# Performance work log

Measured on AMD Instinct MI355X. Metric: run time of the kernel, lower is better.

Reference implementation:

```python
import jax, jax.numpy as jnp
import numpy as np


def setup_inputs() -> dict:
    key = jax.random.key(0)
    kq, kk, kv = jax.random.split(key, 3)
    B, H, S, D = 2, 16, 2048, 64
    q = jax.random.normal(kq, (B, H, S, D), dtype=jnp.float32)
    k = jax.random.normal(kk, (B, H, S, D), dtype=jnp.float32)
    v = jax.random.normal(kv, (B, H, S, D), dtype=jnp.float32)
    return {"q": q, "k": k, "v": v}


def reference(q, k, v):
    # q,k,v: [B,H,S,D]; causal=True
    B, H, S, D = q.shape
    scale = D ** (-0.5)
    scores = jnp.einsum("bhsd,bhtd->bhst", q, k) * scale  # [B,H,S,S]
    causal_mask = jnp.triu(jnp.ones((S, S), dtype=bool), k=1)
    scores = jnp.where(causal_mask, -jnp.inf, scores)
    weights = jax.nn.softmax(scores, axis=-1)
    return jnp.einsum("bhst,bhtd->bhsd", weights, v)
```

## Files before the change

kernel.cpp:

```cpp
#include <hip/hip_runtime.h>
#include <hip/hip_bf16.h>


typedef unsigned int u32;
typedef unsigned short u16;
typedef unsigned long long u64;
typedef __attribute__((ext_vector_type(8))) short short8;
typedef __attribute__((ext_vector_type(4))) float f32x4;

#define DEV static __device__ __forceinline__

constexpr int S_ = 2048, D_ = 64;
constexpr int ELEMS = 2 * 16 * S_ * D_;
constexpr float SCL = 0.125f * 1.44269504089f;

DEV u16 f2bf(float f) {
  u32 u = __builtin_bit_cast(u32, f);
  u += 0x7fffu + ((u >> 16) & 1u);
  return (u16)(u >> 16);
}
DEV u32 pk2(float lo, float hi) { return (u32)f2bf(lo) | ((u32)f2bf(hi) << 16); }
DEV u64 pk4(float4 v) { return (u64)pk2(v.x, v.y) | ((u64)pk2(v.z, v.w) << 32); }

struct Q4 { u32 w[4]; };
struct P2 { u64 a, b; };

__global__ __launch_bounds__(256)
void convbf(const float* __restrict__ src, u16* __restrict__ dst, int n4) {
  int i = blockIdx.x * blockDim.x + threadIdx.x;
  const int stride = gridDim.x * blockDim.x;
  for (; i < n4; i += stride) {
    float4 v = ((const float4*)src)[i];
    ((u64*)dst)[i] = pk4(v);
  }
}

__global__ __launch_bounds__(256, 2)
void fattn(const float* __restrict__ Qg, const u16* __restrict__ Kbf,
           const u16* __restrict__ Vbf, float* __restrict__ Og)
{
  __shared__ __align__(16) u16 Kl[64 * 64];
  __shared__ __align__(16) u16 Vt[64 * 68];
  __shared__ __align__(16) u16 Pl[4][16 * 72];

  const int tid  = threadIdx.x;
  const int wid  = tid >> 6;
  const int lane = tid & 63;
  const int c    = lane & 15;
  const int g    = lane >> 4;

  const int n  = blockIdx.x;
  const int bh = n & 31;
  const int p  = n >> 5;
  const int qbs[2] = {31 - p, p};

  const float* Qb = Qg  + (size_t)bh * S_ * D_;
  const u16*   Kb = Kbf + (size_t)bh * S_ * D_;
  const u16*   Vb = Vbf + (size_t)bh * S_ * D_;
  float*       Ob = Og  + (size_t)bh * S_ * D_;

  char* Kbyte = (char*)Kl;
  char* Vbyte = (char*)Vt;
  char* Pbyte = (char*)(Pl[wid]);

  const int m16  = (tid & 7) * 16;
  const int rK0  = tid >> 3;
  const int rK1  = rK0 + 32;
  const int cf4  = tid & 15;
  const int d0   = cf4 * 4;
  const int kvl0 = 2 * (tid >> 4);
  const int kvl1 = kvl0 + 32;
  short8 pkA, pkB;
  u64 pva0, pvb0, pva1, pvb1;

#define ISSUE(T) do {                                                   \
    const u16* Kt_ = Kb + (size_t)(T) * 64 * D_;                        \
    const u16* Vg_ = Vb + (size_t)(T) * 64 * D_;                        \
    pkA  = *(const short8*)((const char*)Kt_ + rK0 * 128 + m16);        \
    pkB  = *(const short8*)((const char*)Kt_ + rK1 * 128 + m16);        \
    pva0 = *(const u64*)(Vg_ + (size_t)(kvl0    ) * D_ + d0);           \
    pvb0 = *(const u64*)(Vg_ + (size_t)(kvl0 + 1) * D_ + d0);           \
    pva1 = *(const u64*)(Vg_ + (size_t)(kvl1    ) * D_ + d0);           \
    pvb1 = *(const u64*)(Vg_ + (size_t)(kvl1 + 1) * D_ + d0);           \
  } while (0)

  ISSUE(0);

  for (int sp = 0; sp < 2; ++sp) {
    const int qb = qbs[sp];
    const int q0 = qb * 64;
    const int ntiles = qb + 1;

    const int qrow = q0 + wid * 16 + c;
    short8 qf[2];
    for (int kc = 0; kc < 2; ++kc) {
      const float* qp = Qb + (size_t)qrow * D_ + kc * 32 + 8 * g;
      float4 x = *(const float4*)qp;
      float4 y = *(const float4*)(qp + 4);
      Q4 q;
      q.w[0] = pk2(x.x * SCL, x.y * SCL);
      q.w[1] = pk2(x.z * SCL, x.w * SCL);
      q.w[2] = pk2(y.x * SCL, y.y * SCL);
      q.w[3] = pk2(y.z * SCL, y.w * SCL);
      qf[kc] = __builtin_bit_cast(short8, q);
    }

    f32x4 oa[4];
    for (int nd = 0; nd < 4; ++nd) oa[nd] = f32x4{0.f, 0.f, 0.f, 0.f};
    float mrow[4], lrow[4];
    for (int i = 0; i < 4; ++i) { mrow[i] = -__builtin_inff(); lrow[i] = 0.f; }

    for (int t = 0; t < ntiles; ++t) {
      const int kv0 = t * 64;
      __syncthreads();

      {
        *(short8*)(Kbyte + rK0 * 128 + (m16 ^ ((rK0 & 7) << 4))) = pkA;
        *(short8*)(Kbyte + rK1 * 128 + (m16 ^ ((rK1 & 7) << 4))) = pkB;
        u32 a0 = (u32)pva0, a1 = (u32)(pva0 >> 32);
        u32 b0 = (u32)pvb0, b1 = (u32)(pvb0 >> 32);
        *(u32*)(Vbyte + (d0 + 0) * 136 + kvl0 * 2) = (a0 & 0xffffu) | (b0 << 16);
        *(u32*)(Vbyte + (d0 + 1) * 136 + kvl0 * 2) = (a0 >> 16) | (b0 & 0xffff0000u);
        *(u32*)(Vbyte + (d0 + 2) * 136 + kvl0 * 2) = (a1 & 0xffffu) | (b1 << 16);
        *(u32*)(Vbyte + (d0 + 3) * 136 + kvl0 * 2) = (a1 >> 16) | (b1 & 0xffff0000u);
        a0 = (u32)pva1; a1 = (u32)(pva1 >> 32);
        b0 = (u32)pvb1; b1 = (u32)(pvb1 >> 32);
        *(u32*)(Vbyte + (d0 + 0) * 136 + kvl1 * 2) = (a0 & 0xffffu) | (b0 << 16);
        *(u32*)(Vbyte + (d0 + 1) * 136 + kvl1 * 2) = (a0 >> 16) | (b0 & 0xffff0000u);
        *(u32*)(Vbyte + (d0 + 2) * 136 + kvl1 * 2) = (a1 & 0xffffu) | (b1 << 16);
        *(u32*)(Vbyte + (d0 + 3) * 136 + kvl1 * 2) = (a1 >> 16) | (b1 & 0xffff0000u);
      }

      if (t + 1 < ntiles) ISSUE(t + 1);
      else if (sp == 0)   ISSUE(0);

      asm volatile("s_waitcnt lgkmcnt(0)" ::: "memory");
      __builtin_amdgcn_s_barrier();
      asm volatile("" ::: "memory");

      f32x4 sa[4];
      for (int nn = 0; nn < 4; ++nn) {
        sa[nn] = f32x4{0.f, 0.f, 0.f, 0.f};
        const int rowk = nn * 16 + c;
        const int base = rowk * 128;
        const int swz  = (rowk & 7) << 4;
        for (int kc = 0; kc < 2; ++kc) {
          short8 kf = *(const short8*)(Kbyte + base + ((kc * 64 + 16 * g) ^ swz));
          sa[nn] = __builtin_amdgcn_mfma_f32_16x16x32_bf16(qf[kc], kf, sa[nn], 0, 0, 0);
        }
      }

      const bool diag = (t == ntiles - 1);
      float pp[4][4];
      for (int i = 0; i < 4; ++i) {
        const int qg_ = q0 + wid * 16 + 4 * g + i;
        float s0v = sa[0][i], s1v = sa[1][i], s2v = sa[2][i], s3v = sa[3][i];
        if (diag) {
          if (kv0 +  0 + c > qg_) s0v = -__builtin_inff();
          if (kv0 + 16 + c > qg_) s1v = -__builtin_inff();
          if (kv0 + 32 + c > qg_) s2v = -__builtin_inff();
          if (kv0 + 48 + c > qg_) s3v = -__builtin_inff();
        }
        float mx = fmaxf(fmaxf(s0v, s1v), fmaxf(s2v, s3v));
        mx = fmaxf(mx, __shfl_xor(mx, 1));
        mx = fmaxf(mx, __shfl_xor(mx, 2));
        mx = fmaxf(mx, __shfl_xor(mx, 4));
        mx = fmaxf(mx, __shfl_xor(mx, 8));
        if (!__all(mx <= mrow[i] + 8.0f)) {
          const float nm = fmaxf(mrow[i], mx);
          const float al = exp2f(mrow[i] - nm);
          mrow[i] = nm;
          lrow[i] *= al;
          oa[0][i] *= al; oa[1][i] *= al; oa[2][i] *= al; oa[3][i] *= al;
        }
        const float m_ = mrow[i];
        float p0 = exp2f(s0v - m_), p1 = exp2f(s1v - m_);
        float p2 = exp2f(s2v - m_), p3 = exp2f(s3v - m_);
        pp[0][i] = p0; pp[1][i] = p1; pp[2][i] = p2; pp[3][i] = p3;
        float ls = p0 + p1 + p2 + p3;
        ls += __shfl_xor(ls, 1);
        ls += __shfl_xor(ls, 2);
        ls += __shfl_xor(ls, 4);
        ls += __shfl_xor(ls, 8);
        lrow[i] += ls;
      }

      for (int nn = 0; nn < 4; ++nn)
        for (int i = 0; i < 4; ++i)
          *(u16*)(Pbyte + ((4 * g + i) * 72 + nn * 16 + c) * 2) = f2bf(pp[nn][i]);

      for (int kc = 0; kc < 2; ++kc) {
        short8 af = *(const short8*)(Pbyte + c * 144 + kc * 64 + 16 * g);
        for (int nd = 0; nd < 4; ++nd) {
          const int d = nd * 16 + c;
          P2 pv;
          pv.a = *(const u64*)(Vbyte + d * 136 + kc * 64 + 16 * g);
          pv.b = *(const u64*)(Vbyte + d * 136 + kc * 64 + 16 * g + 8);
          short8 vf = __builtin_bit_cast(short8, pv);
          oa[nd] = __builtin_amdgcn_mfma_f32_16x16x32_bf16(af, vf, oa[nd], 0, 0, 0);
        }
      }
    }

    for (int i = 0; i < 4; ++i) {
      const float rl = 1.f / lrow[i];
      float* op = Ob + (size_t)(q0 + wid * 16 + 4 * g + i) * D_ + c;
      op[0]  = oa[0][i] * rl;
      op[16] = oa[1][i] * rl;
      op[32] = oa[2][i] * rl;
      op[48] = oa[3][i] * rl;
    }
  }
}

__global__ __launch_bounds__(256, 4)
void fattn_fb(const float* __restrict__ Qg, const float* __restrict__ Kg,
              const float* __restrict__ Vg, float* __restrict__ Og)
{
  __shared__ __align__(16) u16 Kl[64 * 64];
  __shared__ __align__(16) u16 Vt[64 * 68];
  __shared__ __align__(16) u16 Pl[4][16 * 72];

  const int tid  = threadIdx.x;
  const int wid  = tid >> 6;
  const int lane = tid & 63;
  const int c    = lane & 15;
  const int g    = lane >> 4;

  const int n  = blockIdx.x;
  const int j  = n & 255, kq = n >> 8;
  const int b5 = j & 31,  r3 = j >> 5;
  const int bh = kq * 8 + r3;
  int qb;
  switch (kq) {
    case 0:  qb = b5;              break;
    case 1:  qb = 31 - b5;         break;
    case 2:  qb = (b5 + 16) & 31;  break;
    default: qb = (15 - b5) & 31;  break;
  }
  const int q0 = qb * 64;
  const int ntiles = qb + 1;

  const float* Qb = Qg + (size_t)bh * S_ * D_;
  const float* Kb = Kg + (size_t)bh * S_ * D_;
  const float* Vb = Vg + (size_t)bh * S_ * D_;
  float*       Ob = Og + (size_t)bh * S_ * D_;

  char* Kbyte = (char*)Kl;
  char* Vbyte = (char*)Vt;
  char* Pbyte = (char*)(Pl[wid]);

  const int qrow = q0 + wid * 16 + c;
  short8 qf[2];
  for (int kc = 0; kc < 2; ++kc) {
    const float* qp = Qb + (size_t)qrow * D_ + kc * 32 + 8 * g;
    float4 x = *(const float4*)qp;
    float4 y = *(const float4*)(qp + 4);
    Q4 q;
    q.w[0] = pk2(x.x * SCL, x.y * SCL);
    q.w[1] = pk2(x.z * SCL, x.w * SCL);
    q.w[2] = pk2(y.x * SCL, y.y * SCL);
    q.w[3] = pk2(y.z * SCL, y.w * SCL);
    qf[kc] = __builtin_bit_cast(short8, q);
  }

  f32x4 oa[4];
  for (int nd = 0; nd < 4; ++nd) oa[nd] = f32x4{0.f, 0.f, 0.f, 0.f};
  float mrow[4], lrow[4];
  for (int i = 0; i < 4; ++i) { mrow[i] = -__builtin_inff(); lrow[i] = 0.f; }

  const int cf4  = tid & 15;
  const int krow = tid >> 4;
  const int d0   = cf4 * 4;
  float4 pk0, pk1, pk2v, pk3, pa0, pb0, pa1, pb1;

#define ISSUEF(T) do {                                                    \
    const float* Kt_ = Kb + (size_t)(T) * 64 * D_;                        \
    const float* Vg_ = Vb + (size_t)(T) * 64 * D_;                        \
    pk0 = *(const float4*)(Kt_ + (size_t)(krow     ) * D_ + d0);          \
    pk1 = *(const float4*)(Kt_ + (size_t)(krow + 16) * D_ + d0);          \
    pk2v = *(const float4*)(Kt_ + (size_t)(krow + 32) * D_ + d0);         \
    pk3 = *(const float4*)(Kt_ + (size_t)(krow + 48) * D_ + d0);          \
    const float* s0_ = Vg_ + (size_t)(2 * krow     ) * D_ + d0;           \
    const float* s1_ = Vg_ + (size_t)(2 * krow + 32) * D_ + d0;           \
    pa0 = *(const float4*)s0_;  pb0 = *(const float4*)(s0_ + D_);         \
    pa1 = *(const float4*)s1_;  pb1 = *(const float4*)(s1_ + D_);         \
  } while (0)

  ISSUEF(0);

  for (int t = 0; t < ntiles; ++t) {
    const int kv0 = t * 64;
    __syncthreads();
    {
      const int r0 = krow, r1 = krow + 16, r2 = krow + 32, r3r = krow + 48;
      *(u64*)(Kbyte + r0  * 128 + ((cf4 * 8) ^ ((r0  & 7) << 4))) = pk4(pk0);
      *(u64*)(Kbyte + r1  * 128 + ((cf4 * 8) ^ ((r1  & 7) << 4))) = pk4(pk1);
      *(u64*)(Kbyte + r2  * 128 + ((cf4 * 8) ^ ((r2  & 7) << 4))) = pk4(pk2v);
      *(u64*)(Kbyte + r3r * 128 + ((cf4 * 8) ^ ((r3r & 7) << 4))) = pk4(pk3);
      const int kvl0 = 2 * krow, kvl1 = 2 * krow + 32;
      *(u32*)(Vbyte + (d0 + 0) * 136 + kvl0 * 2) = pk2(pa0.x, pb0.x);
      *(u32*)(Vbyte + (d0 + 1) * 136 + kvl0 * 2) = pk2(pa0.y, pb0.y);
      *(u32*)(Vbyte + (d0 + 2) * 136 + kvl0 * 2) = pk2(pa0.z, pb0.z);
      *(u32*)(Vbyte + (d0 + 3) * 136 + kvl0 * 2) = pk2(pa0.w, pb0.w);
      *(u32*)(Vbyte + (d0 + 0) * 136 + kvl1 * 2) = pk2(pa1.x, pb1.x);
      *(u32*)(Vbyte + (d0 + 1) * 136 + kvl1 * 2) = pk2(pa1.y, pb1.y);
      *(u32*)(Vbyte + (d0 + 2) * 136 + kvl1 * 2) = pk2(pa1.z, pb1.z);
      *(u32*)(Vbyte + (d0 + 3) * 136 + kvl1 * 2) = pk2(pa1.w, pb1.w);
    }
    if (t + 1 < ntiles) ISSUEF(t + 1);
    asm volatile("s_waitcnt lgkmcnt(0)" ::: "memory");
    __builtin_amdgcn_s_barrier();
    asm volatile("" ::: "memory");

    f32x4 sa[4];
    for (int nn = 0; nn < 4; ++nn) {
      sa[nn] = f32x4{0.f, 0.f, 0.f, 0.f};
      const int rowk = nn * 16 + c;
      const int base = rowk * 128;
      const int swz  = (rowk & 7) << 4;
      for (int kc = 0; kc < 2; ++kc) {
        short8 kf = *(const short8*)(Kbyte + base + ((kc * 64 + 16 * g) ^ swz));
        sa[nn] = __builtin_amdgcn_mfma_f32_16x16x32_bf16(qf[kc], kf, sa[nn], 0, 0, 0);
      }
    }

    const bool diag = (t == ntiles - 1);
    float pp[4][4];
    for (int i = 0; i < 4; ++i) {
      const int qg_ = q0 + wid * 16 + 4 * g + i;
      float s0v = sa[0][i], s1v = sa[1][i], s2v = sa[2][i], s3v = sa[3][i];
      if (diag) {
        if (kv0 +  0 + c > qg_) s0v = -__builtin_inff();
        if (kv0 + 16 + c > qg_) s1v = -__builtin_inff();
        if (kv0 + 32 + c > qg_) s2v = -__builtin_inff();
        if (kv0 + 48 + c > qg_) s3v = -__builtin_inff();
      }
      float mx = fmaxf(fmaxf(s0v, s1v), fmaxf(s2v, s3v));
      mx = fmaxf(mx, __shfl_xor(mx, 1));
      mx = fmaxf(mx, __shfl_xor(mx, 2));
      mx = fmaxf(mx, __shfl_xor(mx, 4));
      mx = fmaxf(mx, __shfl_xor(mx, 8));
      const float nm = fmaxf(mrow[i], mx);
      const float al = exp2f(mrow[i] - nm);
      mrow[i] = nm;
      float p0 = exp2f(s0v - nm), p1 = exp2f(s1v - nm);
      float p2 = exp2f(s2v - nm), p3 = exp2f(s3v - nm);
      pp[0][i] = p0; pp[1][i] = p1; pp[2][i] = p2; pp[3][i] = p3;
      float ls = p0 + p1 + p2 + p3;
      ls += __shfl_xor(ls, 1);
      ls += __shfl_xor(ls, 2);
      ls += __shfl_xor(ls, 4);
      ls += __shfl_xor(ls, 8);
      lrow[i] = lrow[i] * al + ls;
      oa[0][i] *= al; oa[1][i] *= al; oa[2][i] *= al; oa[3][i] *= al;
    }

    for (int nn = 0; nn < 4; ++nn)
      for (int i = 0; i < 4; ++i)
        *(u16*)(Pbyte + ((4 * g + i) * 72 + nn * 16 + c) * 2) = f2bf(pp[nn][i]);

    for (int kc = 0; kc < 2; ++kc) {
      short8 af = *(const short8*)(Pbyte + c * 144 + kc * 64 + 16 * g);
      for (int nd = 0; nd < 4; ++nd) {
        const int d = nd * 16 + c;
        P2 pv;
        pv.a = *(const u64*)(Vbyte + d * 136 + kc * 64 + 16 * g);
        pv.b = *(const u64*)(Vbyte + d * 136 + kc * 64 + 16 * g + 8);
        short8 vf = __builtin_bit_cast(short8, pv);
        oa[nd] = __builtin_amdgcn_mfma_f32_16x16x32_bf16(af, vf, oa[nd], 0, 0, 0);
      }
    }
  }

  for (int i = 0; i < 4; ++i) {
    const float rl = 1.f / lrow[i];
    float* op = Ob + (size_t)(q0 + wid * 16 + 4 * g + i) * D_ + c;
    op[0]  = oa[0][i] * rl;
    op[16] = oa[1][i] * rl;
    op[32] = oa[2][i] * rl;
    op[48] = oa[3][i] * rl;
  }
}

extern "C" void kernel_launch(void* const* d_in, const int* in_sizes, int n_in,
                              void* d_out, int out_size, void* d_ws, size_t ws_size,
                              hipStream_t stream) {
  const float* q = (const float*)d_in[0];
  const float* k = (const float*)d_in[1];
  const float* v = (const float*)d_in[2];
  float* o = (float*)d_out;

  const size_t need = (size_t)2 * ELEMS * sizeof(u16);
  if (ws_size >= need) {
    u16* kbf = (u16*)d_ws;
    u16* vbf = kbf + ELEMS;
    const int n4 = ELEMS / 4;
    convbf<<<1024, 256, 0, stream>>>(k, kbf, n4);
    convbf<<<1024, 256, 0, stream>>>(v, vbf, n4);
    fattn<<<512, 256, 0, stream>>>(q, kbf, vbf, o);
  } else {
    fattn_fb<<<1024, 256, 0, stream>>>(q, k, v, o);
  }
}
```

Before: 174.9 us.

## Split KV tile across two wave halves with 512-thread blocks and merge partial softmax

Doubles the block to 8 waves: each group of four waves handles half of every 64-key tile (32 keys), so each wave does half the QK and PV MFMAs per tile. The two halves keep separate running max and sum, and their partial outputs are merged at the end through shared memory reused from the K/V buffers. V is now stored with an XOR swizzle instead of padding, and P is packed with v_cvt_pk_bf16_f32. A finite mask value replaces -inf so fully masked halves stay safe. The change adds an extra merge phase and two barriers per query block, and the higher thread count per CU may cost registers.

```diff
diff --git a/kernel.cpp b/kernel.cpp
--- a/kernel.cpp
+++ b/kernel.cpp
@@ -13,6 +13,7 @@
 constexpr int S_ = 2048, D_ = 64;
 constexpr int ELEMS = 2 * 16 * S_ * D_;
 constexpr float SCL = 0.125f * 1.44269504089f;
+constexpr float MASKV = -1.0e30f;
 
 DEV u16 f2bf(float f) {
   u32 u = __builtin_bit_cast(u32, f);
@@ -35,24 +36,27 @@
   }
 }
 
-__global__ __launch_bounds__(256, 2)
+DEV int vswz(int d) { return (((d & 7) ^ ((d >> 3) & 7)) << 4); }
+
+__global__ __launch_bounds__(512, 4)
 void fattn(const float* __restrict__ Qg, const u16* __restrict__ Kbf,
            const u16* __restrict__ Vbf, float* __restrict__ Og)
 {
   __shared__ __align__(16) u16 Kl[64 * 64];
-  __shared__ __align__(16) u16 Vt[64 * 68];
-  __shared__ __align__(16) u16 Pl[4][16 * 72];
+  __shared__ __align__(16) u16 Vt[64 * 64];
+  __shared__ __align__(16) u16 Pl[8][16 * 40];
 
   const int tid  = threadIdx.x;
   const int wid  = tid >> 6;
   const int lane = tid & 63;
   const int c    = lane & 15;
   const int g    = lane >> 4;
+  const int qg   = wid & 3;
+  const int h    = wid >> 2;
 
   const int n  = blockIdx.x;
   const int bh = n & 31;
   const int p  = n >> 5;
-  const int qbs[2] = {31 - p, p};
 
   const float* Qb = Qg  + (size_t)bh * S_ * D_;
   const u16*   Kb = Kbf + (size_t)bh * S_ * D_;
@@ -61,37 +65,31 @@
 
   char* Kbyte = (char*)Kl;
   char* Vbyte = (char*)Vt;
-  char* Pbyte = (char*)(Pl[wid]);
-
-  const int m16  = (tid & 7) * 16;
-  const int rK0  = tid >> 3;
-  const int rK1  = rK0 + 32;
-  const int cf4  = tid & 15;
-  const int d0   = cf4 * 4;
-  const int kvl0 = 2 * (tid >> 4);
-  const int kvl1 = kvl0 + 32;
-  short8 pkA, pkB;
-  u64 pva0, pvb0, pva1, pvb1;
-
-#define ISSUE(T) do {                                                   \
-    const u16* Kt_ = Kb + (size_t)(T) * 64 * D_;                        \
-    const u16* Vg_ = Vb + (size_t)(T) * 64 * D_;                        \
-    pkA  = *(const short8*)((const char*)Kt_ + rK0 * 128 + m16);        \
-    pkB  = *(const short8*)((const char*)Kt_ + rK1 * 128 + m16);        \
-    pva0 = *(const u64*)(Vg_ + (size_t)(kvl0    ) * D_ + d0);           \
-    pvb0 = *(const u64*)(Vg_ + (size_t)(kvl0 + 1) * D_ + d0);           \
-    pva1 = *(const u64*)(Vg_ + (size_t)(kvl1    ) * D_ + d0);           \
-    pvb1 = *(const u64*)(Vg_ + (size_t)(kvl1 + 1) * D_ + d0);           \
+  char* Pbyte = (char*)Pl + wid * 1280;
+
+  const int krow = tid >> 3;
+  const int km16 = (tid & 7) * 16;
+  const int p5   = tid >> 4;
+  const int d0v  = (tid & 15) * 4;
+  short8 pkA;
+  u64 pv0, pv1;
+
+#define ISSUE(T) do {                                                        \
+    pkA = *(const short8*)((const char*)Kb + (size_t)(T) * 8192 +            \
+                           krow * 128 + km16);                               \
+    const u16* Vg_ = Vb + (size_t)(T) * 4096;                                \
+    pv0 = *(const u64*)(Vg_ + (2 * p5    ) * 64 + d0v);                      \
+    pv1 = *(const u64*)(Vg_ + (2 * p5 + 1) * 64 + d0v);                      \
   } while (0)
 
   ISSUE(0);
 
   for (int sp = 0; sp < 2; ++sp) {
-    const int qb = qbs[sp];
+    const int qb = (sp == 0) ? (31 - p) : p;
     const int q0 = qb * 64;
     const int ntiles = qb + 1;
 
-    const int qrow = q0 + wid * 16 + c;
+    const int qrow = q0 + qg * 16 + c;
     short8 qf[2];
     for (int kc = 0; kc < 2; ++kc) {
       const float* qp = Qb + (size_t)qrow * D_ + kc * 32 + 8 * g;
@@ -108,27 +106,22 @@
     f32x4 oa[4];
     for (int nd = 0; nd < 4; ++nd) oa[nd] = f32x4{0.f, 0.f, 0.f, 0.f};
     float mrow[4], lrow[4];
-    for (int i = 0; i < 4; ++i) { mrow[i] = -__builtin_inff(); lrow[i] = 0.f; }
+    for (int i = 0; i < 4; ++i) { mrow[i] = MASKV; lrow[i] = 0.f; }
 
     for (int t = 0; t < ntiles; ++t) {
       const int kv0 = t * 64;
       __syncthreads();
 
       {
-        *(short8*)(Kbyte + rK0 * 128 + (m16 ^ ((rK0 & 7) << 4))) = pkA;
-        *(short8*)(Kbyte + rK1 * 128 + (m16 ^ ((rK1 & 7) << 4))) = pkB;
-        u32 a0 = (u32)pva0, a1 = (u32)(pva0 >> 32);
-        u32 b0 = (u32)pvb0, b1 = (u32)(pvb0 >> 32);
-        *(u32*)(Vbyte + (d0 + 0) * 136 + kvl0 * 2) = (a0 & 0xffffu) | (b0 << 16);
-        *(u32*)(Vbyte + (d0 + 1) * 136 + kvl0 * 2) = (a0 >> 16) | (b0 & 0xffff0000u);
-        *(u32*)(Vbyte + (d0 + 2) * 136 + kvl0 * 2) = (a1 & 0xffffu) | (b1 << 16);
-        *(u32*)(Vbyte + (d0 + 3) * 136 + kvl0 * 2) = (a1 >> 16) | (b1 & 0xffff0000u);
-        a0 = (u32)pva1; a1 = (u32)(pva1 >> 32);
-        b0 = (u32)pvb1; b1 = (u32)(pvb1 >> 32);
-        *(u32*)(Vbyte + (d0 + 0) * 136 + kvl1 * 2) = (a0 & 0xffffu) | (b0 << 16);
-        *(u32*)(Vbyte + (d0 + 1) * 136 + kvl1 * 2) = (a0 >> 16) | (b0 & 0xffff0000u);
-        *(u32*)(Vbyte + (d0 + 2) * 136 + kvl1 * 2) = (a1 & 0xffffu) | (b1 << 16);
-        *(u32*)(Vbyte + (d0 + 3) * 136 + kvl1 * 2) = (a1 >> 16) | (b1 & 0xffff0000u);
+        *(short8*)(Kbyte + krow * 128 + (km16 ^ ((krow & 7) << 4))) = pkA;
+        const u32 lo0 = (u32)pv0, hi0 = (u32)(pv0 >> 32);
+        const u32 lo1 = (u32)pv1, hi1 = (u32)(pv1 >> 32);
+        const int cb = 4 * p5;
+        int d = d0v;
+        *(u32*)(Vbyte + d * 128 + (cb ^ vswz(d))) = (lo0 & 0xffffu) | (lo1 << 16); ++d;
+        *(u32*)(Vbyte + d * 128 + (cb ^ vswz(d))) = (lo0 >> 16) | (lo1 & 0xffff0000u); ++d;
+        *(u32*)(Vbyte + d * 128 + (cb ^ vswz(d))) = (hi0 & 0xffffu) | (hi1 << 16); ++d;
+        *(u32*)(Vbyte + d * 128 + (cb ^ vswz(d))) = (hi0 >> 16) | (hi1 & 0xffff0000u);
       }
 
       if (t + 1 < ntiles) ISSUE(t + 1);
@@ -138,10 +131,10 @@
       __builtin_amdgcn_s_barrier();
       asm volatile("" ::: "memory");
 
-      f32x4 sa[4];
-      for (int nn = 0; nn < 4; ++nn) {
+      f32x4 sa[2];
+      for (int nn = 0; nn < 2; ++nn) {
         sa[nn] = f32x4{0.f, 0.f, 0.f, 0.f};
-        const int rowk = nn * 16 + c;
+        const int rowk = 32 * h + 16 * nn + c;
         const int base = rowk * 128;
         const int swz  = (rowk & 7) << 4;
         for (int kc = 0; kc < 2; ++kc) {
@@ -151,17 +144,15 @@
       }
 
       const bool diag = (t == ntiles - 1);
-      float pp[4][4];
       for (int i = 0; i < 4; ++i) {
-        const int qg_ = q0 + wid * 16 + 4 * g + i;
-        float s0v = sa[0][i], s1v = sa[1][i], s2v = sa[2][i], s3v = sa[3][i];
+        const int qabs = q0 + qg * 16 + 4 * g + i;
+        float s0v = sa[0][i], s1v = sa[1][i];
         if (diag) {
-          if (kv0 +  0 + c > qg_) s0v = -__builtin_inff();
-          if (kv0 + 16 + c > qg_) s1v = -__builtin_inff();
-          if (kv0 + 32 + c > qg_) s2v = -__builtin_inff();
-          if (kv0 + 48 + c > qg_) s3v = -__builtin_inff();
-        }
-        float mx = fmaxf(fmaxf(s0v, s1v), fmaxf(s2v, s3v));
+          const int kvb = kv0 + 32 * h;
+          if (kvb +  0 + c > qabs) s0v = MASKV;
+          if (kvb + 16 + c > qabs) s1v = MASKV;
+        }
+        float mx = fmaxf(s0v, s1v);
         mx = fmaxf(mx, __shfl_xor(mx, 1));
         mx = fmaxf(mx, __shfl_xor(mx, 2));
         mx = fmaxf(mx, __shfl_xor(mx, 4));
@@ -174,41 +165,64 @@
           oa[0][i] *= al; oa[1][i] *= al; oa[2][i] *= al; oa[3][i] *= al;
         }
         const float m_ = mrow[i];
-        float p0 = exp2f(s0v - m_), p1 = exp2f(s1v - m_);
-        float p2 = exp2f(s2v - m_), p3 = exp2f(s3v - m_);
-        pp[0][i] = p0; pp[1][i] = p1; pp[2][i] = p2; pp[3][i] = p3;
-        float ls = p0 + p1 + p2 + p3;
-        ls += __shfl_xor(ls, 1);
-        ls += __shfl_xor(ls, 2);
-        ls += __shfl_xor(ls, 4);
-        ls += __shfl_xor(ls, 8);
-        lrow[i] += ls;
-      }
-
-      for (int nn = 0; nn < 4; ++nn)
-        for (int i = 0; i < 4; ++i)
-          *(u16*)(Pbyte + ((4 * g + i) * 72 + nn * 16 + c) * 2) = f2bf(pp[nn][i]);
-
-      for (int kc = 0; kc < 2; ++kc) {
-        short8 af = *(const short8*)(Pbyte + c * 144 + kc * 64 + 16 * g);
+        const float p0 = exp2f(s0v - m_);
+        const float p1 = exp2f(s1v - m_);
+        lrow[i] += p0 + p1;
+        u32 pk;
+        asm("v_cvt_pk_bf16_f32 %0, %1, %2" : "=v"(pk) : "v"(p0), "v"(p1));
+        char* pr = Pbyte + (4 * g + i) * 80;
+        *(u16*)(pr + 2 * c)      = (u16)pk;
+        *(u16*)(pr + 32 + 2 * c) = (u16)(pk >> 16);
+      }
+
+      {
+        short8 af = *(const short8*)(Pbyte + c * 80 + 16 * g);
         for (int nd = 0; nd < 4; ++nd) {
           const int d = nd * 16 + c;
-          P2 pv;
-          pv.a = *(const u64*)(Vbyte + d * 136 + kc * 64 + 16 * g);
-          pv.b = *(const u64*)(Vbyte + d * 136 + kc * 64 + 16 * g + 8);
-          short8 vf = __builtin_bit_cast(short8, pv);
+          short8 vf = *(const short8*)(Vbyte + d * 128 + ((64 * h + 16 * g) ^ vswz(d)));
           oa[nd] = __builtin_amdgcn_mfma_f32_16x16x32_bf16(af, vf, oa[nd], 0, 0, 0);
         }
       }
     }
 
     for (int i = 0; i < 4; ++i) {
-      const float rl = 1.f / lrow[i];
-      float* op = Ob + (size_t)(q0 + wid * 16 + 4 * g + i) * D_ + c;
-      op[0]  = oa[0][i] * rl;
-      op[16] = oa[1][i] * rl;
-      op[32] = oa[2][i] * rl;
-      op[48] = oa[3][i] * rl;
+      float ls = lrow[i];
+      ls += __shfl_xor(ls, 1);
+      ls += __shfl_xor(ls, 2);
+      ls += __shfl_xor(ls, 4);
+      ls += __shfl_xor(ls, 8);
+      lrow[i] = ls;
+    }
+    __syncthreads();
+    float* ob = (qg < 2) ? ((float*)Kl + qg * 1024) : ((float*)Vt + (qg - 2) * 1024);
+    if (h == 1) {
+      float* mb = (float*)Pbyte;
+      if (c == 0) {
+        for (int i = 0; i < 4; ++i) {
+          mb[4 * g + i]      = mrow[i];
+          mb[16 + 4 * g + i] = lrow[i];
+        }
+      }
+      for (int i = 0; i < 4; ++i)
+        for (int nd = 0; nd < 4; ++nd)
+          ob[(4 * g + i) * 64 + ((nd * 16 + c) ^ (g << 4))] = oa[nd][i];
+    }
+    __syncthreads();
+    if (h == 0) {
+      const float* mb1 = (const float*)((char*)Pl + (4 + qg) * 1280);
+      for (int i = 0; i < 4; ++i) {
+        const float m1 = mb1[4 * g + i];
+        const float l1 = mb1[16 + 4 * g + i];
+        const float m  = fmaxf(mrow[i], m1);
+        const float a0 = exp2f(mrow[i] - m);
+        const float a1 = exp2f(m1 - m);
+        const float rl = 1.0f / (lrow[i] * a0 + l1 * a1);
+        float* op = Ob + (size_t)(q0 + qg * 16 + 4 * g + i) * D_;
+        for (int nd = 0; nd < 4; ++nd) {
+          const float o1 = ob[(4 * g + i) * 64 + ((nd * 16 + c) ^ (g << 4))];
+          op[nd * 16 + c] = (oa[nd][i] * a0 + o1 * a1) * rl;
+        }
+      }
     }
   }
 }
@@ -398,7 +412,7 @@
     const int n4 = ELEMS / 4;
     convbf<<<1024, 256, 0, stream>>>(k, kbf, n4);
     convbf<<<1024, 256, 0, stream>>>(v, vbf, n4);
-    fattn<<<512, 256, 0, stream>>>(q, kbf, vbf, o);
+    fattn<<<512, 512, 0, stream>>>(q, kbf, vbf, o);
   } else {
     fattn_fb<<<1024, 256, 0, stream>>>(q, k, v, o);
   }
```

Result: slower. 181.7 us (+3.9%).
